# Kernel tuning notes

Measured on AMD Instinct MI355X. Metric: run time of the kernel, lower is better.

## Reference

```python
import jax, jax.numpy as jnp
import numpy as np

N = 50000
C_IN = 64
C_OUT = 64
K = 16
EPS = 1e-5


def _bn(x, g, b, m, v):
    # eval-mode BatchNorm1d over last dim
    return (x - m) * jax.lax.rsqrt(v + EPS) * g + b


def setup_inputs() -> dict:
    key = jax.random.key(0)
    ks = jax.random.split(key, 24)
    def lin(i, fan_in, fan_out):
        s = 1.0 / np.sqrt(fan_in)
        W = jax.random.uniform(ks[i], (fan_in, fan_out), jnp.float32, -s, s)
        b = jax.random.uniform(ks[i + 1], (fan_out,), jnp.float32, -s, s)
        return W, b
    Wq, bq = lin(0, C_IN, C_OUT)
    Wk, bk = lin(2, C_IN, C_OUT)
    Wv, bv = lin(4, C_IN, C_OUT)
    Wp, b_p = lin(6, 3, C_OUT)
    Wg1, bg1 = lin(8, C_OUT, C_OUT)
    Wg2, bg2 = lin(10, C_OUT, C_OUT)
    Wo, bo = lin(12, C_OUT, C_OUT)
    def bn_params(i):
        g = jax.random.uniform(ks[i], (C_OUT,), jnp.float32, 0.5, 1.5)
        b = jax.random.normal(ks[i + 1], (C_OUT,), jnp.float32) * 0.1
        m = jax.random.normal(ks[i + 2], (C_OUT,), jnp.float32) * 0.1
        v = jax.random.uniform(ks[i + 3], (C_OUT,), jnp.float32, 0.5, 1.5)
        return g, b, m, v
    bnp_g, bnp_b, bnp_m, bnp_v = bn_params(14)
    bng_g, bng_b, bng_m, bng_v = bn_params(18)
    points = jax.random.normal(ks[22], (N, 3), jnp.float32)
    features = jax.random.normal(ks[23], (N, C_IN), jnp.float32)
    grouped_indices = jax.random.randint(jax.random.fold_in(key, 7), (N, K), 0, N, jnp.int64 if jax.config.jax_enable_x64 else jnp.int32)
    return dict(points=points, features=features, grouped_indices=grouped_indices,
                Wq=Wq, bq=bq, Wk=Wk, bk=bk, Wv=Wv, bv=bv, Wp=Wp, b_p=b_p,
                bnp_g=bnp_g, bnp_b=bnp_b, bnp_m=bnp_m, bnp_v=bnp_v,
                Wg1=Wg1, bg1=bg1, bng_g=bng_g, bng_b=bng_b, bng_m=bng_m, bng_v=bng_v,
                Wg2=Wg2, bg2=bg2, Wo=Wo, bo=bo)


def reference(points, features, grouped_indices,
              Wq, bq, Wk, bk, Wv, bv, Wp, b_p,
              bnp_g, bnp_b, bnp_m, bnp_v,
              Wg1, bg1, bng_g, bng_b, bng_m, bng_v,
              Wg2, bg2, Wo, bo):
    q = features @ Wq + bq                      # (N, C)
    k = features @ Wk + bk
    v = features @ Wv + bv
    gpts = points[grouped_indices]              # (N, K, 3) gather
    gk = k[grouped_indices]                     # (N, K, C)
    gv = v[grouped_indices]                     # (N, K, C)
    rel = gpts - points[:, None, :]             # (N, K, 3)
    p = jax.nn.relu(_bn(rel @ Wp + b_p, bnp_g, bnp_b, bnp_m, bnp_v))  # (N, K, C)
    a = q[:, None, :] - gk + p                  # (N, K, C)
    h = jax.nn.relu(_bn(a @ Wg1 + bg1, bng_g, bng_b, bng_m, bng_v)) @ Wg2 + bg2
    attn = jax.nn.softmax(h, axis=1)            # softmax over neighbor axis
    out = jnp.sum((gv + p) * attn, axis=1) @ Wo + bo  # (N, C)
    return out
```

## Files before the change

kernel.cpp:

```cpp
#include <hip/hip_runtime.h>
#include <hip/hip_bf16.h>

#define EPSV 1e-5f
#define TW 4
#define TPW 4
#define SPD 76

typedef __attribute__((ext_vector_type(8))) short s8v;
typedef __attribute__((ext_vector_type(4))) float f4v;

struct InP {
  const float *points, *features; const int* gidx;
  const float *Wq,*bq,*Wk,*bk,*Wv,*bv,*Wp,*b_p;
  const float *bnp_g,*bnp_b,*bnp_m,*bnp_v;
  const float *Wg1,*bg1,*bng_g,*bng_b,*bng_m,*bng_v;
  const float *Wg2,*bg2,*Wo,*bo;
  float* out; int N;
};
struct WS {
  unsigned short *qW1;
  unsigned short *kvT;
  unsigned short *WAf, *Wkf, *Wvf, *W1f, *W2f, *Wof;
  unsigned short *Wpf;
  float *bq1F, *bpF;
};

__device__ __forceinline__ unsigned short f2bf(float x){
  __hip_bfloat16 h = __float2bfloat16(x);
  unsigned short u; __builtin_memcpy(&u, &h, 2); return u;
}
__device__ __forceinline__ float bf2f(unsigned short s){
  union{unsigned u; float f;} c; c.u = ((unsigned)s) << 16; return c.f;
}
__device__ __forceinline__ unsigned pk2(float x, float y){
  __hip_bfloat162 h = __float22bfloat162_rn(make_float2(x, y));
  unsigned u; __builtin_memcpy(&u, &h, 4); return u;
}
__device__ __forceinline__ s8v pack8(f4v x0, f4v x1){
  s8v r;
  ((unsigned*)&r)[0] = pk2(x0[0], x0[1]);
  ((unsigned*)&r)[1] = pk2(x0[2], x0[3]);
  ((unsigned*)&r)[2] = pk2(x1[0], x1[1]);
  ((unsigned*)&r)[3] = pk2(x1[2], x1[3]);
  return r;
}
__device__ __forceinline__ s8v sub8bf(s8v p, s8v k){
  s8v r;
  #pragma unroll
  for (int t = 0; t < 4; t++){
    float a0 = bf2f((unsigned short)p[2*t+0]) - bf2f((unsigned short)k[2*t+0]);
    float a1 = bf2f((unsigned short)p[2*t+1]) - bf2f((unsigned short)k[2*t+1]);
    ((unsigned*)&r)[t] = pk2(a0, a1);
  }
  return r;
}

__global__ void __launch_bounds__(256) prep_kernel(InP P, WS W){
  const int g = blockIdx.x*256 + threadIdx.x;
  const int e = g >> 3, j = g & 7;
  const int f = e >> 6, L = e & 63;
  const int ks = f & 1, nt = f >> 1;
  const int n = nt*16 + (L & 15);
  const int k = ks*32 + ((L >> 4) << 3) + j;
  const float sg = P.bng_g[n] * rsqrtf(P.bng_v[n] + EPSV);
  W.W1f[e*8+j] = f2bf(P.Wg1[k*64+n] * sg);
  W.W2f[e*8+j] = f2bf(P.Wg2[k*64+n]);
  W.Wof[e*8+j] = f2bf(P.Wo [k*64+n]);
  W.Wkf[e*8+j] = f2bf(P.Wk [k*64+n]);
  W.Wvf[e*8+j] = f2bf(P.Wv [k*64+n]);
  float acc = 0.f;
  #pragma unroll 8
  for (int d = 0; d < 64; d++) acc += P.Wq[k*64+d] * P.Wg1[d*64+n];
  W.WAf[e*8+j] = f2bf(acc * sg);
  if (g < 2048){
    int ep = g >> 3;
    int ntp = ep >> 6, Lp = ep & 63;
    int np_ = ntp*16 + (Lp & 15);
    int kp = ((Lp >> 4) << 3) + j;
    float sp = P.bnp_g[np_] * rsqrtf(P.bnp_v[np_] + EPSV);
    W.Wpf[ep*8+j] = f2bf(kp < 3 ? P.Wp[kp*64+np_]*sp : 0.f);
  }
  if (g < 64){
    float sgt = P.bng_g[g] * rsqrtf(P.bng_v[g] + EPSV);
    float spt = P.bnp_g[g] * rsqrtf(P.bnp_v[g] + EPSV);
    float acc2 = 0.f;
    for (int d = 0; d < 64; d++) acc2 += P.bq[d] * P.Wg1[d*64+g];
    W.bq1F[g] = acc2*sgt + P.bg1[g]*sgt + P.bng_b[g] - P.bng_m[g]*sgt;
    W.bpF[g]  = P.b_p[g]*spt + P.bnp_b[g] - P.bnp_m[g]*spt;
  }
}

__global__ void __launch_bounds__(256) qkv_kernel(InP P, WS W){
  const int tid = threadIdx.x;
  const int wid = tid >> 6, l = tid & 63;
  const int cl = l & 15, q = l >> 4;
  const int TILES = (P.N + 15) >> 4;
  const int task = blockIdx.x * TW + wid;
  if (task >= TILES) return;
  const int i0 = task * 16;
  int row = i0 + cl; if (row > P.N - 1) row = P.N - 1;
  const float* fr = P.features + (size_t)row*64 + q*8;
  f4v x0 = *(const f4v*)fr;
  f4v x1 = *(const f4v*)(fr + 4);
  s8v fa0 = pack8(x0, x1);
  x0 = *(const f4v*)(fr + 32);
  x1 = *(const f4v*)(fr + 36);
  s8v fa1 = pack8(x0, x1);

  auto doMat = [&](const unsigned short* Bf_, const float* biasPtr,
                   unsigned short* outPtr, int stride){
    const s8v* Bf = (const s8v*)Bf_;
    #pragma unroll
    for (int nt = 0; nt < 4; nt++){
      float bn = biasPtr[nt*16 + cl];
      f4v ci = { bn, bn, bn, bn };
      f4v c = __builtin_amdgcn_mfma_f32_16x16x32_bf16(fa0, Bf[(2*nt+0)*64 + l], ci, 0, 0, 0);
      c = __builtin_amdgcn_mfma_f32_16x16x32_bf16(fa1, Bf[(2*nt+1)*64 + l], c, 0, 0, 0);
      #pragma unroll
      for (int r = 0; r < 4; r++){
        int rg = i0 + q*4 + r;
        if (rg < P.N) outPtr[(size_t)rg*stride + nt*16 + cl] = f2bf(c[r]);
      }
    }
  };
  doMat(W.WAf, W.bq1F, W.qW1,      64);
  doMat(W.Wkf, P.bk,   W.kvT,     128);
  doMat(W.Wvf, P.bv,   W.kvT + 64,128);
}

__global__ void __launch_bounds__(256, 2) main_kernel(InP P, WS W){
  __shared__ __align__(16) unsigned short Sp[TW][2][16*SPD];
  __shared__ __align__(16) unsigned short PreB[TW][TPW*SPD];
  __shared__ __align__(16) int sI[TW][TPW*16];
  const int tid = threadIdx.x;
  const int wid = tid >> 6, l = tid & 63;
  const int cl = l & 15, q = l >> 4;
  const int TILES = (P.N + TPW - 1) / TPW;
  const int task = blockIdx.x * TW + wid;
  if (task >= TILES) return;
  const int i0 = task * TPW;
  unsigned short* PreBw = PreB[wid];
  int* sIw = sI[wid];

  {
    long base = (long)i0*16 + l;
    long maxb = (long)P.N*16 - 1;
    if (base > maxb) base = maxb;
    sIw[l] = P.gidx[base];
  }

  s8v w1f[8], w2f[8], wpf[4];
  {
    const s8v* W1p = (const s8v*)W.W1f;
    const s8v* W2p = (const s8v*)W.W2f;
    const s8v* Wpp = (const s8v*)W.Wpf;
    #pragma unroll
    for (int f = 0; f < 8; f++){ w1f[f] = W1p[f*64 + l]; w2f[f] = W2p[f*64 + l]; }
    #pragma unroll
    for (int f = 0; f < 4; f++) wpf[f] = Wpp[f*64 + l];
  }
  float bp4[4], b24[4];
  #pragma unroll
  for (int nt = 0; nt < 4; nt++){ bp4[nt] = W.bpF[nt*16 + cl]; b24[nt] = P.bg2[nt*16 + cl]; }

  int nidx = sIw[cl];
  s8v ngk0, ngk1;
  {
    const s8v* kv = (const s8v*)(W.kvT + (size_t)nidx*128);
    ngk0 = kv[q]; ngk1 = kv[4+q];
  }
  float ngx=0.f, ngy=0.f, ngz=0.f;
  if (l < 16){ const float* gp = P.points + (size_t)nidx*3; ngx=gp[0]; ngy=gp[1]; ngz=gp[2]; }
  float ncx = P.points[(size_t)i0*3+0];
  float ncy = P.points[(size_t)i0*3+1];
  float ncz = P.points[(size_t)i0*3+2];
  float nq0, nq1, nq2, nq3;
  {
    const unsigned short* qr = W.qW1 + (size_t)i0*64;
    nq0 = bf2f(qr[cl]); nq1 = bf2f(qr[16+cl]); nq2 = bf2f(qr[32+cl]); nq3 = bf2f(qr[48+cl]);
  }

  #pragma unroll 2
  for (int pt = 0; pt < TPW; pt++){
    unsigned short* Spw = Sp[wid][pt & 1];
    s8v gk0=ngk0, gk1=ngk1;
    float gx=ngx, gy=ngy, gz=ngz, cx=ncx, cy=ncy, cz=ncz;
    float qc0=nq0, qc1=nq1, qc2=nq2, qc3=nq3;
    const bool valid = (i0 + pt < P.N);

    unsigned short vv[16];
    {
      int4 vidx = *(const int4*)&sIw[pt*16 + q*4];
      #pragma unroll
      for (int r = 0; r < 4; r++){
        const unsigned short* vb = W.kvT + (size_t)vidx[r]*128 + 64 + cl;
        #pragma unroll
        for (int nt = 0; nt < 4; nt++) vv[nt*4+r] = vb[nt*16];
      }
    }

    s8v ap;
    ((unsigned*)&ap)[0] = pk2(gx-cx, gy-cy);
    ((unsigned*)&ap)[1] = pk2(gz-cz, 0.f);
    ((unsigned*)&ap)[2] = 0u; ((unsigned*)&ap)[3] = 0u;
    f4v pc[4];
    #pragma unroll
    for (int nt = 0; nt < 4; nt++){
      f4v ci = { bp4[nt], bp4[nt], bp4[nt], bp4[nt] };
      pc[nt] = __builtin_amdgcn_mfma_f32_16x16x32_bf16(ap, wpf[nt], ci, 0, 0, 0);
    }
    #pragma unroll
    for (int nt = 0; nt < 4; nt++){
      #pragma unroll
      for (int r = 0; r < 4; r++){
        pc[nt][r] = fmaxf(pc[nt][r], 0.f);
        Spw[(q*4+r)*SPD + nt*16 + cl] = f2bf(pc[nt][r]);
      }
    }

    {
      int np = (pt + 1) & (TPW-1);
      nidx = sIw[np*16 + cl];
      const s8v* kv = (const s8v*)(W.kvT + (size_t)nidx*128);
      ngk0 = kv[q]; ngk1 = kv[4+q];
      if (l < 16){ const float* gp = P.points + (size_t)nidx*3; ngx=gp[0]; ngy=gp[1]; ngz=gp[2]; }
      int ii = i0 + np; if (ii > P.N - 1) ii = P.N - 1;
      ncx = P.points[(size_t)ii*3+0];
      ncy = P.points[(size_t)ii*3+1];
      ncz = P.points[(size_t)ii*3+2];
      const unsigned short* qr = W.qW1 + (size_t)ii*64;
      nq0 = bf2f(qr[cl]); nq1 = bf2f(qr[16+cl]); nq2 = bf2f(qr[32+cl]); nq3 = bf2f(qr[48+cl]);
    }

    s8v af0, af1;
    {
      s8v p0 = *(const s8v*)&Spw[cl*SPD + q*8];
      s8v p1 = *(const s8v*)&Spw[cl*SPD + 32 + q*8];
      af0 = sub8bf(p0, gk0);
      af1 = sub8bf(p1, gk1);
    }

    f4v tc[4];
    #pragma unroll
    for (int nt = 0; nt < 4; nt++){
      float qcn = (nt==0) ? qc0 : (nt==1) ? qc1 : (nt==2) ? qc2 : qc3;
      f4v ci = { qcn, qcn, qcn, qcn };
      tc[nt] = __builtin_amdgcn_mfma_f32_16x16x32_bf16(af0, w1f[2*nt+0], ci, 0, 0, 0);
      tc[nt] = __builtin_amdgcn_mfma_f32_16x16x32_bf16(af1, w1f[2*nt+1], tc[nt], 0, 0, 0);
      #pragma unroll
      for (int r = 0; r < 4; r++) tc[nt][r] = fmaxf(tc[nt][r], 0.f);
    }

    #pragma unroll
    for (int nt = 0; nt < 4; nt++)
      #pragma unroll
      for (int r = 0; r < 4; r++)
        Spw[(q*4+r)*SPD + nt*16 + cl] = f2bf(tc[nt][r]);
    s8v tf0 = *(const s8v*)&Spw[cl*SPD + q*8];
    s8v tf1 = *(const s8v*)&Spw[cl*SPD + 32 + q*8];

    f4v hc[4];
    #pragma unroll
    for (int nt = 0; nt < 4; nt++){
      f4v ci = { b24[nt], b24[nt], b24[nt], b24[nt] };
      hc[nt] = __builtin_amdgcn_mfma_f32_16x16x32_bf16(tf0, w2f[2*nt+0], ci, 0, 0, 0);
      hc[nt] = __builtin_amdgcn_mfma_f32_16x16x32_bf16(tf1, w2f[2*nt+1], hc[nt], 0, 0, 0);
    }

    float pre4[4];
    #pragma unroll
    for (int nt = 0; nt < 4; nt++){
      float s = 0.f, acc = 0.f;
      #pragma unroll
      for (int r = 0; r < 4; r++){
        float e2 = __expf(hc[nt][r]);
        s += e2;
        acc = fmaf(e2, bf2f(vv[nt*4+r]) + pc[nt][r], acc);
      }
      s += __shfl_xor(s, 16, 64);
      s += __shfl_xor(s, 32, 64);
      acc += __shfl_xor(acc, 16, 64);
      acc += __shfl_xor(acc, 32, 64);
      pre4[nt] = acc * __builtin_amdgcn_rcpf(s);
    }
    if (valid){
      float sa = (l & 16) ? pre4[1] : pre4[0];
      float sb = (l & 16) ? pre4[3] : pre4[2];
      PreBw[pt*SPD + l] = f2bf((l & 32) ? sb : sa);
    }
  }

  s8v wof[8];
  {
    const s8v* Wop = (const s8v*)W.Wof;
    #pragma unroll
    for (int f = 0; f < 8; f++) wof[f] = Wop[f*64 + l];
  }
  s8v ef0 = *(const s8v*)&PreBw[(cl & (TPW-1))*SPD + q*8];
  s8v ef1 = *(const s8v*)&PreBw[(cl & (TPW-1))*SPD + 32 + q*8];
  #pragma unroll
  for (int nt = 0; nt < 4; nt++){
    float bn = P.bo[nt*16 + cl];
    f4v ci = { bn, bn, bn, bn };
    f4v oc = __builtin_amdgcn_mfma_f32_16x16x32_bf16(ef0, wof[2*nt+0], ci, 0, 0, 0);
    oc = __builtin_amdgcn_mfma_f32_16x16x32_bf16(ef1, wof[2*nt+1], oc, 0, 0, 0);
    #pragma unroll
    for (int r = 0; r < 4; r++){
      int ro = q*4 + r;
      int rg = i0 + ro;
      if (ro < TPW && rg < P.N) P.out[(size_t)rg*64 + nt*16 + cl] = oc[r];
    }
  }
}

extern "C" void kernel_launch(void* const* d_in, const int* in_sizes, int n_in,
                              void* d_out, int out_size, void* d_ws, size_t ws_size,
                              hipStream_t stream){
  InP P;
  P.points   = (const float*)d_in[0];
  P.features = (const float*)d_in[1];
  P.gidx     = (const int*)d_in[2];
  P.Wq  = (const float*)d_in[3];  P.bq  = (const float*)d_in[4];
  P.Wk  = (const float*)d_in[5];  P.bk  = (const float*)d_in[6];
  P.Wv  = (const float*)d_in[7];  P.bv  = (const float*)d_in[8];
  P.Wp  = (const float*)d_in[9];  P.b_p = (const float*)d_in[10];
  P.bnp_g = (const float*)d_in[11]; P.bnp_b = (const float*)d_in[12];
  P.bnp_m = (const float*)d_in[13]; P.bnp_v = (const float*)d_in[14];
  P.Wg1 = (const float*)d_in[15]; P.bg1 = (const float*)d_in[16];
  P.bng_g = (const float*)d_in[17]; P.bng_b = (const float*)d_in[18];
  P.bng_m = (const float*)d_in[19]; P.bng_v = (const float*)d_in[20];
  P.Wg2 = (const float*)d_in[21]; P.bg2 = (const float*)d_in[22];
  P.Wo  = (const float*)d_in[23]; P.bo  = (const float*)d_in[24];
  P.out = (float*)d_out;
  const int N = in_sizes[0] / 3;
  P.N = N;

  WS W;
  char* w = (char*)d_ws;
  W.qW1 = (unsigned short*)w; w += (size_t)N*64*2;
  W.kvT = (unsigned short*)w; w += (size_t)N*128*2;
  W.WAf = (unsigned short*)w; w += 8*64*8*2;
  W.Wkf = (unsigned short*)w; w += 8*64*8*2;
  W.Wvf = (unsigned short*)w; w += 8*64*8*2;
  W.W1f = (unsigned short*)w; w += 8*64*8*2;
  W.W2f = (unsigned short*)w; w += 8*64*8*2;
  W.Wof = (unsigned short*)w; w += 8*64*8*2;
  W.Wpf = (unsigned short*)w; w += 4*64*8*2;
  W.bq1F = (float*)w; w += 256;
  W.bpF  = (float*)w; w += 256;

  const int TILES16 = (N + 15) / 16;
  const int grid16 = (TILES16 + TW - 1) / TW;
  const int TILESM = (N + TPW - 1) / TPW;
  const int gridM = (TILESM + TW - 1) / TW;
  hipLaunchKernelGGL(prep_kernel, dim3(16),     dim3(256), 0, stream, P, W);
  hipLaunchKernelGGL(qkv_kernel,  dim3(grid16), dim3(256), 0, stream, P, W);
  hipLaunchKernelGGL(main_kernel, dim3(gridM),  dim3(256), 0, stream, P, W);
}
```

Baseline: 209.0 us.

## Fold key projection through Wg1 and apply it as MFMA accumulator init

Precomputes k·Wg1 (with the BN scale) in the qkv kernel, so the main kernel no longer forms q−k+p in bf16 before the first MLP layer. It subtracts the projected key as the MFMA accumulator initializer, gathered per row in the same layout as v. It also raises points per wave from 4 to 8 and vectorizes the index load to int2. The goal is to remove the per-element bf16 subtraction and repacking, at the cost of more scattered 2-byte gathers for k and a different rounding path, since p is now rounded before the Wg1 product instead of after the subtraction.

```diff
diff --git a/kernel.cpp b/kernel.cpp
--- a/kernel.cpp
+++ b/kernel.cpp
@@ -3,7 +3,7 @@
 
 #define EPSV 1e-5f
 #define TW 4
-#define TPW 4
+#define TPW 8
 #define SPD 76
 
 typedef __attribute__((ext_vector_type(8))) short s8v;
@@ -22,7 +22,7 @@
   unsigned short *kvT;
   unsigned short *WAf, *Wkf, *Wvf, *W1f, *W2f, *Wof;
   unsigned short *Wpf;
-  float *bq1F, *bpF;
+  float *bq1F, *bpF, *bk1F;
 };
 
 __device__ __forceinline__ unsigned short f2bf(float x){
@@ -42,16 +42,6 @@
   ((unsigned*)&r)[1] = pk2(x0[2], x0[3]);
   ((unsigned*)&r)[2] = pk2(x1[0], x1[1]);
   ((unsigned*)&r)[3] = pk2(x1[2], x1[3]);
-  return r;
-}
-__device__ __forceinline__ s8v sub8bf(s8v p, s8v k){
-  s8v r;
-  #pragma unroll
-  for (int t = 0; t < 4; t++){
-    float a0 = bf2f((unsigned short)p[2*t+0]) - bf2f((unsigned short)k[2*t+0]);
-    float a1 = bf2f((unsigned short)p[2*t+1]) - bf2f((unsigned short)k[2*t+1]);
-    ((unsigned*)&r)[t] = pk2(a0, a1);
-  }
   return r;
 }
 
@@ -66,12 +56,16 @@
   W.W1f[e*8+j] = f2bf(P.Wg1[k*64+n] * sg);
   W.W2f[e*8+j] = f2bf(P.Wg2[k*64+n]);
   W.Wof[e*8+j] = f2bf(P.Wo [k*64+n]);
-  W.Wkf[e*8+j] = f2bf(P.Wk [k*64+n]);
   W.Wvf[e*8+j] = f2bf(P.Wv [k*64+n]);
-  float acc = 0.f;
+  float acc = 0.f, acck = 0.f;
   #pragma unroll 8
-  for (int d = 0; d < 64; d++) acc += P.Wq[k*64+d] * P.Wg1[d*64+n];
-  W.WAf[e*8+j] = f2bf(acc * sg);
+  for (int d = 0; d < 64; d++){
+    float w1 = P.Wg1[d*64+n];
+    acc  += P.Wq[k*64+d] * w1;
+    acck += P.Wk[k*64+d] * w1;
+  }
+  W.WAf[e*8+j] = f2bf(acc  * sg);
+  W.Wkf[e*8+j] = f2bf(acck * sg);
   if (g < 2048){
     int ep = g >> 3;
     int ntp = ep >> 6, Lp = ep & 63;
@@ -83,9 +77,14 @@
   if (g < 64){
     float sgt = P.bng_g[g] * rsqrtf(P.bng_v[g] + EPSV);
     float spt = P.bnp_g[g] * rsqrtf(P.bnp_v[g] + EPSV);
-    float acc2 = 0.f;
-    for (int d = 0; d < 64; d++) acc2 += P.bq[d] * P.Wg1[d*64+g];
+    float acc2 = 0.f, acck2 = 0.f;
+    for (int d = 0; d < 64; d++){
+      float w1 = P.Wg1[d*64+g];
+      acc2  += P.bq[d] * w1;
+      acck2 += P.bk[d] * w1;
+    }
     W.bq1F[g] = acc2*sgt + P.bg1[g]*sgt + P.bng_b[g] - P.bng_m[g]*sgt;
+    W.bk1F[g] = acck2*sgt;
     W.bpF[g]  = P.b_p[g]*spt + P.bnp_b[g] - P.bnp_m[g]*spt;
   }
 }
@@ -124,7 +123,7 @@
     }
   };
   doMat(W.WAf, W.bq1F, W.qW1,      64);
-  doMat(W.Wkf, P.bk,   W.kvT,     128);
+  doMat(W.Wkf, W.bk1F, W.kvT,     128);
   doMat(W.Wvf, P.bv,   W.kvT + 64,128);
 }
 
@@ -143,10 +142,11 @@
   int* sIw = sI[wid];
 
   {
-    long base = (long)i0*16 + l;
-    long maxb = (long)P.N*16 - 1;
+    long base = (long)i0*16 + l*2;
+    long maxb = (long)P.N*16 - 2;
     if (base > maxb) base = maxb;
-    sIw[l] = P.gidx[base];
+    int2 gi = *(const int2*)(P.gidx + base);
+    *(int2*)&sIw[l*2] = gi;
   }
 
   s8v w1f[8], w2f[8], wpf[4];
@@ -163,14 +163,11 @@
   #pragma unroll
   for (int nt = 0; nt < 4; nt++){ bp4[nt] = W.bpF[nt*16 + cl]; b24[nt] = P.bg2[nt*16 + cl]; }
 
-  int nidx = sIw[cl];
-  s8v ngk0, ngk1;
-  {
-    const s8v* kv = (const s8v*)(W.kvT + (size_t)nidx*128);
-    ngk0 = kv[q]; ngk1 = kv[4+q];
-  }
   float ngx=0.f, ngy=0.f, ngz=0.f;
-  if (l < 16){ const float* gp = P.points + (size_t)nidx*3; ngx=gp[0]; ngy=gp[1]; ngz=gp[2]; }
+  {
+    int nidx = sIw[cl];
+    if (l < 16){ const float* gp = P.points + (size_t)nidx*3; ngx=gp[0]; ngy=gp[1]; ngz=gp[2]; }
+  }
   float ncx = P.points[(size_t)i0*3+0];
   float ncy = P.points[(size_t)i0*3+1];
   float ncz = P.points[(size_t)i0*3+2];
@@ -183,19 +180,21 @@
   #pragma unroll 2
   for (int pt = 0; pt < TPW; pt++){
     unsigned short* Spw = Sp[wid][pt & 1];
-    s8v gk0=ngk0, gk1=ngk1;
     float gx=ngx, gy=ngy, gz=ngz, cx=ncx, cy=ncy, cz=ncz;
-    float qc0=nq0, qc1=nq1, qc2=nq2, qc3=nq3;
+    float qcn4[4] = { nq0, nq1, nq2, nq3 };
     const bool valid = (i0 + pt < P.N);
 
-    unsigned short vv[16];
+    unsigned short kw[16], vv[16];
     {
       int4 vidx = *(const int4*)&sIw[pt*16 + q*4];
       #pragma unroll
       for (int r = 0; r < 4; r++){
-        const unsigned short* vb = W.kvT + (size_t)vidx[r]*128 + 64 + cl;
+        const unsigned short* vb = W.kvT + (size_t)vidx[r]*128 + cl;
         #pragma unroll
-        for (int nt = 0; nt < 4; nt++) vv[nt*4+r] = vb[nt*16];
+        for (int nt = 0; nt < 4; nt++){
+          kw[nt*4+r] = vb[nt*16];
+          vv[nt*4+r] = vb[64 + nt*16];
+        }
       }
     }
 
@@ -220,9 +219,7 @@
 
     {
       int np = (pt + 1) & (TPW-1);
-      nidx = sIw[np*16 + cl];
-      const s8v* kv = (const s8v*)(W.kvT + (size_t)nidx*128);
-      ngk0 = kv[q]; ngk1 = kv[4+q];
+      int nidx = sIw[np*16 + cl];
       if (l < 16){ const float* gp = P.points + (size_t)nidx*3; ngx=gp[0]; ngy=gp[1]; ngz=gp[2]; }
       int ii = i0 + np; if (ii > P.N - 1) ii = P.N - 1;
       ncx = P.points[(size_t)ii*3+0];
@@ -232,19 +229,16 @@
       nq0 = bf2f(qr[cl]); nq1 = bf2f(qr[16+cl]); nq2 = bf2f(qr[32+cl]); nq3 = bf2f(qr[48+cl]);
     }
 
-    s8v af0, af1;
-    {
-      s8v p0 = *(const s8v*)&Spw[cl*SPD + q*8];
-      s8v p1 = *(const s8v*)&Spw[cl*SPD + 32 + q*8];
-      af0 = sub8bf(p0, gk0);
-      af1 = sub8bf(p1, gk1);
-    }
+    s8v af0 = *(const s8v*)&Spw[cl*SPD + q*8];
+    s8v af1 = *(const s8v*)&Spw[cl*SPD + 32 + q*8];
 
     f4v tc[4];
     #pragma unroll
     for (int nt = 0; nt < 4; nt++){
-      float qcn = (nt==0) ? qc0 : (nt==1) ? qc1 : (nt==2) ? qc2 : qc3;
-      f4v ci = { qcn, qcn, qcn, qcn };
+      f4v ci = { qcn4[nt] - bf2f(kw[nt*4+0]),
+                 qcn4[nt] - bf2f(kw[nt*4+1]),
+                 qcn4[nt] - bf2f(kw[nt*4+2]),
+                 qcn4[nt] - bf2f(kw[nt*4+3]) };
       tc[nt] = __builtin_amdgcn_mfma_f32_16x16x32_bf16(af0, w1f[2*nt+0], ci, 0, 0, 0);
       tc[nt] = __builtin_amdgcn_mfma_f32_16x16x32_bf16(af1, w1f[2*nt+1], tc[nt], 0, 0, 0);
       #pragma unroll
@@ -348,6 +342,7 @@
   W.Wpf = (unsigned short*)w; w += 4*64*8*2;
   W.bq1F = (float*)w; w += 256;
   W.bpF  = (float*)w; w += 256;
+  W.bk1F = (float*)w; w += 256;
 
   const int TILES16 = (N + 15) / 16;
   const int grid16 = (TILES16 + TW - 1) / TW;
```

New measurement: 204.1 us. 1.02x faster.
